# Performance work log

Measured on AMD Instinct MI355X. Metric: run time of the kernel, lower is better.

Reference implementation:

```python
import jax, jax.numpy as jnp
import numpy as np

B, V, H, W = 2, 4, 352, 352
R_PIX = H * W
SH_DEGREE = 1
D_SH = (SH_DEGREE + 1) ** 2
SCALE_MIN, SCALE_MAX = 0.5, 15.0
EPS = 1e-8
C0 = 0.28209479177387814  # SH DC basis constant


def quat_to_mat(q):
    # (w, x, y, z) convention, matches pytorch3d quaternion_to_matrix
    w, x, y, z = q[..., 0], q[..., 1], q[..., 2], q[..., 3]
    two_s = 2.0 / jnp.sum(q * q, axis=-1)
    o = jnp.stack([
        1 - two_s * (y * y + z * z), two_s * (x * y - z * w), two_s * (x * z + y * w),
        two_s * (x * y + z * w), 1 - two_s * (x * x + z * z), two_s * (y * z - x * w),
        two_s * (x * z - y * w), two_s * (y * z + x * w), 1 - two_s * (x * x + y * y),
    ], axis=-1)
    return o.reshape(*q.shape[:-1], 3, 3)


def setup_inputs() -> dict:
    key = jax.random.key(0)
    ks = jax.random.split(key, 8)
    # valid c2w extrinsics: random rotation (from unit quaternion) + translation
    q = jax.random.normal(ks[0], (B, V, 4))
    q = q / jnp.linalg.norm(q, axis=-1, keepdims=True)
    Rm = quat_to_mat(q)
    t = jax.random.normal(ks[1], (B, V, 3))
    E = jnp.zeros((B, V, 4, 4))
    E = E.at[..., :3, :3].set(Rm).at[..., :3, 3].set(t).at[..., 3, 3].set(1.0)
    extrinsics = E.reshape(B, V, 1, 1, 1, 4, 4)
    # normalized pinhole intrinsics
    f = jax.random.uniform(ks[2], (B, V, 2), minval=0.8, maxval=1.2)
    K = jnp.zeros((B, V, 3, 3))
    K = K.at[..., 0, 0].set(f[..., 0]).at[..., 1, 1].set(f[..., 1])
    K = K.at[..., 0, 2].set(0.5).at[..., 1, 2].set(0.5).at[..., 2, 2].set(1.0)
    intrinsics = K.reshape(B, V, 1, 1, 1, 3, 3)
    coordinates = jax.random.uniform(ks[3], (B, V, R_PIX, 1, 1, 2))
    depths = jax.random.uniform(ks[4], (B, V, R_PIX, 1, 1), minval=0.5, maxval=10.0)
    opacities = jax.random.uniform(ks[5], (B, V, R_PIX, 1, 1))
    raw_gaussians = jax.random.normal(ks[6], (B, V, R_PIX, 1, 1, 7 + 3 * D_SH))
    input_images = jax.random.uniform(ks[7], (B, V, 3, H, W))
    sh_mask = jnp.ones((D_SH,), jnp.float32)
    for deg in range(1, SH_DEGREE + 1):
        sh_mask = sh_mask.at[deg ** 2:(deg + 1) ** 2].set(0.1 * 0.25 ** deg)
    return {"extrinsics": extrinsics, "intrinsics": intrinsics, "coordinates": coordinates,
            "depths": depths, "opacities": opacities, "raw_gaussians": raw_gaussians,
            "input_images": input_images, "sh_mask": sh_mask}


def reference(extrinsics, intrinsics, coordinates, depths, opacities, raw_gaussians, input_images, sh_mask):
    d_sh = sh_mask.shape[0]
    # split raw gaussians: scales (3), quaternion (4), sh (3*d_sh)
    scales = jnp.clip(jax.nn.softplus(raw_gaussians[..., :3] - 4.0), SCALE_MIN, SCALE_MAX)
    rot = raw_gaussians[..., 3:7]
    rotations = rot / (jnp.linalg.norm(rot, axis=-1, keepdims=True) + EPS)
    sh = raw_gaussians[..., 7:].reshape(*raw_gaussians.shape[:-1], 3, d_sh) * sh_mask
    # inject image colors into the DC SH coefficient
    b, v, c, h, w = input_images.shape
    imgs = input_images.transpose(0, 1, 3, 4, 2).reshape(b, v, h * w, 1, 1, c)
    sh = sh.at[..., 0].add((imgs - 0.5) / C0)  # RGB2SH
    # covariance = R diag(s^2) R^T, then rotate into world frame
    Rq = quat_to_mat(rotations)
    cov = jnp.einsum('...ij,...j,...kj->...ik', Rq, scales * scales, Rq)
    Rc = extrinsics[..., :3, :3]  # (b,v,1,1,1,3,3) c2w rotation
    cov = jnp.einsum('...ij,...jk,...lk->...il', Rc, cov, Rc)
    # unproject rays: d = normalize(K^-1 [x,y,1]), world dir = R d, origin = t
    Kinv = jnp.linalg.inv(intrinsics)
    xy1 = jnp.concatenate([coordinates, jnp.ones_like(coordinates[..., :1])], axis=-1)
    d = jnp.einsum('...ij,...j->...i', Kinv, xy1)
    d = d / jnp.linalg.norm(d, axis=-1, keepdims=True)
    dirs = jnp.einsum('...ij,...j->...i', Rc, d)
    means = jnp.broadcast_to(extrinsics[..., :3, 3], dirs.shape) + dirs * depths[..., None]
    # rotate SH: degree 0 identity; degree 1 Wigner-D = P R P^T with P: (x,y,z)->(y,z,x)
    perm = jnp.array([1, 2, 0])
    D1 = Rc[..., perm[:, None], perm[None, :]]  # (b,v,1,1,1,3,3)
    sh1 = jnp.einsum('...ij,...xj->...xi', D1, sh[..., 1:4])
    harmonics = jnp.concatenate([sh[..., :1], sh1], axis=-1)
    return means, cov, scales, rotations, harmonics, opacities
```

## Files before the change

kernel.cpp:

```cpp
#include <hip/hip_runtime.h>

#define R_PIX 123904
#define NVIEW 8
#define NPIX  (R_PIX * (size_t)NVIEW)

#define OFF_MEANS  ((size_t)0)
#define OFF_COV    ((size_t)2973696)
#define OFF_SCALES ((size_t)11894784)
#define OFF_ROT    ((size_t)14868480)
#define OFF_HARM   ((size_t)18833408)
#define OFF_OPAC   ((size_t)30728192)

__global__ __launch_bounds__(256) void gaussian_adapter_kernel(
    const float* __restrict__ extr,
    const float* __restrict__ intr,
    const float* __restrict__ coords,
    const float* __restrict__ depths,
    const float* __restrict__ opac,
    const float* __restrict__ raw,
    const float* __restrict__ imgs,
    const float* __restrict__ shmask,
    float* __restrict__ out)
{
    const int bv = blockIdx.y;
    const int p  = blockIdx.x * blockDim.x + threadIdx.x;
    const size_t pix = (size_t)bv * R_PIX + p;

    float Rc[3][3], tvec[3];
    {
        const float* E = extr + bv * 16;
        #pragma unroll
        for (int i = 0; i < 3; i++) {
            #pragma unroll
            for (int j = 0; j < 3; j++) Rc[i][j] = E[i * 4 + j];
            tvec[i] = E[i * 4 + 3];
        }
    }
    const float* K = intr + bv * 9;
    const float fx = K[0], cx = K[2];
    const float fy = K[4], cy = K[5];
    float sm[4];
    #pragma unroll
    for (int j = 0; j < 4; j++) sm[j] = shmask[j];

    float rg[19];
    {
        const float* rp = raw + pix * 19;
        #pragma unroll
        for (int i = 0; i < 19; i++) rg[i] = rp[i];
    }

    float sc[3];
    #pragma unroll
    for (int k = 0; k < 3; k++) {
        float xv = rg[k] - 4.0f;
        float sp = fmaxf(xv, 0.0f) + log1pf(expf(-fabsf(xv)));
        sc[k] = fminf(fmaxf(sp, 0.5f), 15.0f);
    }

    float q[4];
    float qn = 0.0f;
    #pragma unroll
    for (int k = 0; k < 4; k++) { q[k] = rg[3 + k]; qn += q[k] * q[k]; }
    const float inorm = 1.0f / (sqrtf(qn) + 1e-8f);
    #pragma unroll
    for (int k = 0; k < 4; k++) q[k] *= inorm;

    float sh[3][4];
    #pragma unroll
    for (int c = 0; c < 3; c++)
        #pragma unroll
        for (int j = 0; j < 4; j++) sh[c][j] = rg[7 + c * 4 + j] * sm[j];
    {
        const float invC0 = 1.0f / 0.28209479177387814f;
        #pragma unroll
        for (int c = 0; c < 3; c++) {
            float im = imgs[((size_t)bv * 3 + c) * R_PIX + p];
            sh[c][0] += (im - 0.5f) * invC0;
        }
    }

    const float qw = q[0], qx = q[1], qy = q[2], qz = q[3];
    const float two_s = 2.0f / (qw * qw + qx * qx + qy * qy + qz * qz);
    float Rq[3][3];
    Rq[0][0] = 1.0f - two_s * (qy * qy + qz * qz);
    Rq[0][1] = two_s * (qx * qy - qz * qw);
    Rq[0][2] = two_s * (qx * qz + qy * qw);
    Rq[1][0] = two_s * (qx * qy + qz * qw);
    Rq[1][1] = 1.0f - two_s * (qx * qx + qz * qz);
    Rq[1][2] = two_s * (qy * qz - qx * qw);
    Rq[2][0] = two_s * (qx * qz - qy * qw);
    Rq[2][1] = two_s * (qy * qz + qx * qw);
    Rq[2][2] = 1.0f - two_s * (qx * qx + qy * qy);

    const float s2[3] = { sc[0] * sc[0], sc[1] * sc[1], sc[2] * sc[2] };
    float cov3[3][3];
    #pragma unroll
    for (int i = 0; i < 3; i++)
        #pragma unroll
        for (int k = 0; k < 3; k++)
            cov3[i][k] = Rq[i][0] * s2[0] * Rq[k][0]
                       + Rq[i][1] * s2[1] * Rq[k][1]
                       + Rq[i][2] * s2[2] * Rq[k][2];
    float M[3][3];
    #pragma unroll
    for (int i = 0; i < 3; i++)
        #pragma unroll
        for (int k = 0; k < 3; k++)
            M[i][k] = Rc[i][0] * cov3[0][k] + Rc[i][1] * cov3[1][k] + Rc[i][2] * cov3[2][k];
    float cov[3][3];
    #pragma unroll
    for (int i = 0; i < 3; i++)
        #pragma unroll
        for (int l = 0; l < 3; l++)
            cov[i][l] = M[i][0] * Rc[l][0] + M[i][1] * Rc[l][1] + M[i][2] * Rc[l][2];

    const float u = coords[pix * 2 + 0];
    const float v = coords[pix * 2 + 1];
    float d0 = (u - cx) / fx;
    float d1 = (v - cy) / fy;
    float d2 = 1.0f;
    {
        const float nrm = sqrtf(d0 * d0 + d1 * d1 + d2 * d2);
        d0 /= nrm; d1 /= nrm; d2 /= nrm;
    }
    float dirs[3];
    #pragma unroll
    for (int i = 0; i < 3; i++)
        dirs[i] = Rc[i][0] * d0 + Rc[i][1] * d1 + Rc[i][2] * d2;

    const float dep = depths[pix];
    float means[3];
    #pragma unroll
    for (int i = 0; i < 3; i++) means[i] = tvec[i] + dirs[i] * dep;

    const int perm[3] = {1, 2, 0};
    float harm[3][4];
    #pragma unroll
    for (int c = 0; c < 3; c++) {
        harm[c][0] = sh[c][0];
        #pragma unroll
        for (int i = 0; i < 3; i++) {
            float acc = 0.0f;
            #pragma unroll
            for (int j = 0; j < 3; j++)
                acc += Rc[perm[i]][perm[j]] * sh[c][1 + j];
            harm[c][1 + i] = acc;
        }
    }

    {
        float* o = out + OFF_MEANS + pix * 3;
        #pragma unroll
        for (int i = 0; i < 3; i++) o[i] = means[i];
    }
    {
        float* o = out + OFF_COV + pix * 9;
        #pragma unroll
        for (int i = 0; i < 3; i++)
            #pragma unroll
            for (int j = 0; j < 3; j++) o[i * 3 + j] = cov[i][j];
    }
    {
        float* o = out + OFF_SCALES + pix * 3;
        #pragma unroll
        for (int i = 0; i < 3; i++) o[i] = sc[i];
    }
    {
        float* o = out + OFF_ROT + pix * 4;
        #pragma unroll
        for (int i = 0; i < 4; i++) o[i] = q[i];
    }
    {
        float* o = out + OFF_HARM + pix * 12;
        #pragma unroll
        for (int c = 0; c < 3; c++)
            #pragma unroll
            for (int j = 0; j < 4; j++) o[c * 4 + j] = harm[c][j];
    }
    out[OFF_OPAC + pix] = opac[pix];
}

extern "C" void kernel_launch(void* const* d_in, const int* in_sizes, int n_in,
                              void* d_out, int out_size, void* d_ws, size_t ws_size,
                              hipStream_t stream) {
    const float* extr   = (const float*)d_in[0];
    const float* intr   = (const float*)d_in[1];
    const float* coords = (const float*)d_in[2];
    const float* depths = (const float*)d_in[3];
    const float* opac   = (const float*)d_in[4];
    const float* raw    = (const float*)d_in[5];
    const float* imgs   = (const float*)d_in[6];
    const float* shmask = (const float*)d_in[7];
    float* out = (float*)d_out;

    dim3 grid(R_PIX / 256, NVIEW);
    dim3 block(256);
    gaussian_adapter_kernel<<<grid, block, 0, stream>>>(
        extr, intr, coords, depths, opac, raw, imgs, shmask, out);
}
```

Measured before the change: 226.7 us.

## Stage raw input and AoS outputs through LDS for coalesced float4 access

Loads each block's 19-float-per-pixel raw parameters into shared memory with coalesced float4 reads, then reads them back per thread. Outputs with stride 3, 9 and 12 (means, cov, scales, harmonics) are written to LDS first and then stored to global memory as coalesced float4 writes. Rotations and coords switch to float4/float2 vector accesses. The goal is to remove strided, uncoalesced global traffic in this bandwidth-bound kernel, in exchange for about 28KB of LDS per block, extra barriers, and possible LDS bank conflicts from the stride-19 and stride-13 reads.

```diff
diff --git a/kernel.cpp b/kernel.cpp
--- a/kernel.cpp
+++ b/kernel.cpp
@@ -5,11 +5,17 @@
 #define NPIX  (R_PIX * (size_t)NVIEW)
 
 #define OFF_MEANS  ((size_t)0)
-#define OFF_COV    ((size_t)2973696)
-#define OFF_SCALES ((size_t)11894784)
-#define OFF_ROT    ((size_t)14868480)
-#define OFF_HARM   ((size_t)18833408)
-#define OFF_OPAC   ((size_t)30728192)
+#define OFF_COV    ((size_t)(3  * NPIX))
+#define OFF_SCALES ((size_t)(12 * NPIX))
+#define OFF_ROT    ((size_t)(15 * NPIX))
+#define OFF_HARM   ((size_t)(19 * NPIX))
+#define OFF_OPAC   ((size_t)(31 * NPIX))
+
+#define MEANS_L  0
+#define COV_L    768
+#define SCALES_L 3072
+#define HARM_L   3840
+#define LDS_DW   7168
 
 __global__ __launch_bounds__(256) void gaussian_adapter_kernel(
     const float* __restrict__ extr,
@@ -22,9 +28,22 @@
     const float* __restrict__ shmask,
     float* __restrict__ out)
 {
-    const int bv = blockIdx.y;
-    const int p  = blockIdx.x * blockDim.x + threadIdx.x;
-    const size_t pix = (size_t)bv * R_PIX + p;
+    const int t   = threadIdx.x;
+    const int bv  = blockIdx.y;
+    const int bp0 = blockIdx.x * 256;
+    const size_t base_pix = (size_t)bv * R_PIX + bp0;
+    const int p   = bp0 + t;
+    const size_t pix = base_pix + t;
+
+    __shared__ __align__(16) float lds[LDS_DW];
+
+    {
+        const float4* g = (const float4*)(raw + base_pix * 19);
+        float4* s = (float4*)lds;
+        #pragma unroll
+        for (int i = 0; i < 4; i++) s[t + 256 * i] = g[t + 256 * i];
+        if (t < 192) s[t + 1024] = g[t + 1024];
+    }
 
     float Rc[3][3], tvec[3];
     {
@@ -43,12 +62,11 @@
     #pragma unroll
     for (int j = 0; j < 4; j++) sm[j] = shmask[j];
 
+    __syncthreads();
+
     float rg[19];
-    {
-        const float* rp = raw + pix * 19;
-        #pragma unroll
-        for (int i = 0; i < 19; i++) rg[i] = rp[i];
-    }
+    #pragma unroll
+    for (int i = 0; i < 19; i++) rg[i] = lds[t * 19 + i];
 
     float sc[3];
     #pragma unroll
@@ -115,8 +133,11 @@
         for (int l = 0; l < 3; l++)
             cov[i][l] = M[i][0] * Rc[l][0] + M[i][1] * Rc[l][1] + M[i][2] * Rc[l][2];
 
-    const float u = coords[pix * 2 + 0];
-    const float v = coords[pix * 2 + 1];
+    float u, v;
+    {
+        const float2 uv = ((const float2*)coords)[pix];
+        u = uv.x; v = uv.y;
+    }
     float d0 = (u - cx) / fx;
     float d1 = (v - cy) / fy;
     float d2 = 1.0f;
@@ -124,15 +145,11 @@
         const float nrm = sqrtf(d0 * d0 + d1 * d1 + d2 * d2);
         d0 /= nrm; d1 /= nrm; d2 /= nrm;
     }
-    float dirs[3];
-    #pragma unroll
-    for (int i = 0; i < 3; i++)
-        dirs[i] = Rc[i][0] * d0 + Rc[i][1] * d1 + Rc[i][2] * d2;
-
     const float dep = depths[pix];
     float means[3];
     #pragma unroll
-    for (int i = 0; i < 3; i++) means[i] = tvec[i] + dirs[i] * dep;
+    for (int i = 0; i < 3; i++)
+        means[i] = tvec[i] + (Rc[i][0] * d0 + Rc[i][1] * d1 + Rc[i][2] * d2) * dep;
 
     const int perm[3] = {1, 2, 0};
     float harm[3][4];
@@ -149,36 +166,53 @@
         }
     }
 
-    {
-        float* o = out + OFF_MEANS + pix * 3;
-        #pragma unroll
-        for (int i = 0; i < 3; i++) o[i] = means[i];
-    }
-    {
-        float* o = out + OFF_COV + pix * 9;
-        #pragma unroll
-        for (int i = 0; i < 3; i++)
-            #pragma unroll
-            for (int j = 0; j < 3; j++) o[i * 3 + j] = cov[i][j];
-    }
-    {
-        float* o = out + OFF_SCALES + pix * 3;
-        #pragma unroll
-        for (int i = 0; i < 3; i++) o[i] = sc[i];
-    }
-    {
-        float* o = out + OFF_ROT + pix * 4;
-        #pragma unroll
-        for (int i = 0; i < 4; i++) o[i] = q[i];
-    }
-    {
-        float* o = out + OFF_HARM + pix * 12;
-        #pragma unroll
-        for (int c = 0; c < 3; c++)
-            #pragma unroll
-            for (int j = 0; j < 4; j++) o[c * 4 + j] = harm[c][j];
-    }
+    ((float4*)(out + OFF_ROT))[pix] = make_float4(q[0], q[1], q[2], q[3]);
     out[OFF_OPAC + pix] = opac[pix];
+
+    __syncthreads();
+
+    #pragma unroll
+    for (int i = 0; i < 3; i++) lds[MEANS_L + t * 3 + i] = means[i];
+    #pragma unroll
+    for (int i = 0; i < 3; i++)
+        #pragma unroll
+        for (int j = 0; j < 3; j++) lds[COV_L + t * 9 + i * 3 + j] = cov[i][j];
+    #pragma unroll
+    for (int i = 0; i < 3; i++) lds[SCALES_L + t * 3 + i] = sc[i];
+    #pragma unroll
+    for (int c = 0; c < 3; c++)
+        #pragma unroll
+        for (int j = 0; j < 4; j++) lds[HARM_L + t * 13 + c * 4 + j] = harm[c][j];
+
+    __syncthreads();
+
+    {
+        float4* g = (float4*)(out + OFF_MEANS + base_pix * 3);
+        const float4* s = (const float4*)(lds + MEANS_L);
+        if (t < 192) g[t] = s[t];
+    }
+    {
+        float4* g = (float4*)(out + OFF_COV + base_pix * 9);
+        const float4* s = (const float4*)(lds + COV_L);
+        g[t] = s[t];
+        g[t + 256] = s[t + 256];
+        if (t < 64) g[t + 512] = s[t + 512];
+    }
+    {
+        float4* g = (float4*)(out + OFF_SCALES + base_pix * 3);
+        const float4* s = (const float4*)(lds + SCALES_L);
+        if (t < 192) g[t] = s[t];
+    }
+    {
+        float4* g = (float4*)(out + OFF_HARM + base_pix * 12);
+        #pragma unroll
+        for (int it = 0; it < 3; it++) {
+            int i = t + 256 * it;
+            int px = i / 3, k = i % 3;
+            const float* s = lds + HARM_L + px * 13 + k * 4;
+            g[i] = make_float4(s[0], s[1], s[2], s[3]);
+        }
+    }
 }
 
 extern "C" void kernel_launch(void* const* d_in, const int* in_sizes, int n_in,
```

Result: no change. 226.0 us (-0.3%).
